# Kernel optimization log

Measured on AMD Instinct MI355X. Metric: run time of the kernel, lower is better.

Reference implementation:

```python
import jax, jax.numpy as jnp
import numpy as np

LN_EPS = 1e-5


def _ln_all_nonbatch(t):
    # torch nn.LayerNorm(t.size()[1:]) created fresh each call: identity affine,
    # normalize jointly over all non-batch dims, biased variance, eps=1e-5.
    axes = tuple(range(1, t.ndim))
    mu = jnp.mean(t, axis=axes, keepdims=True)
    var = jnp.mean(jnp.square(t - mu), axis=axes, keepdims=True)
    return (t - mu) / jnp.sqrt(var + LN_EPS)


def setup_inputs() -> dict:
    key = jax.random.key(0)
    kx, kq, kk, kv = jax.random.split(key, 4)
    B, S, E, d = 32, 1024, 768, 64
    x = jax.random.normal(kx, (B, S, E), dtype=jnp.float32)
    Wq = jax.random.normal(kq, (E, d), dtype=jnp.float32)
    Wk = jax.random.normal(kk, (E, d), dtype=jnp.float32)
    Wv = jax.random.normal(kv, (E, d), dtype=jnp.float32)
    return {"x": x, "Wq": Wq, "Wk": Wk, "Wv": Wv}


def reference(x, Wq, Wk, Wv):
    # x: [B,S,E]; Wq/Wk/Wv: [E,d]
    Q = jnp.einsum('bse,ed->bsd', x, Wq)            # [B,S,d]
    K = jnp.swapaxes(jnp.einsum('bse,ed->bsd', x, Wk), -2, -1)  # [B,d,S]
    V = jnp.einsum('bse,ed->bsd', x, Wv)            # [B,S,d]
    Q = _ln_all_nonbatch(Q)
    K = _ln_all_nonbatch(K)
    V = _ln_all_nonbatch(V)
    d = Q.shape[-1]  # K.shape[1] after transpose == head dim
    scores = jnp.einsum('bsd,bdt->bst', Q, K) / jnp.sqrt(jnp.float32(d))  # [B,S,S]
    attn = jax.nn.softmax(scores, axis=-1)
    return jnp.einsum('bst,btd->bsd', attn, V)      # [B,S,d]
```

## Files before the change

### kernel.cpp

```cpp
#include <hip/hip_runtime.h>
#include <hip/hip_fp16.h>

typedef _Float16 f16x8 __attribute__((ext_vector_type(8)));
typedef _Float16 f16x4 __attribute__((ext_vector_type(4)));
typedef float    f32x4 __attribute__((ext_vector_type(4)));

#define NB   32
#define SEQ  1024
#define EDIM 768
#define HD   64
#define MTOT (NB * SEQ)

__global__ __launch_bounds__(256) void pack_w(const float* __restrict__ Wq,
                                              const float* __restrict__ Wk,
                                              const float* __restrict__ Wv,
                                              _Float16* __restrict__ Wt) {
    int c = blockIdx.x;
    const float* src = (c < 64) ? Wq : (c < 128) ? Wk : Wv;
    int cc = c & 63;
    for (int e = threadIdx.x; e < EDIM; e += 256)
        Wt[(size_t)c * EDIM + e] = (_Float16)src[(size_t)e * HD + cc];
}

__global__ __launch_bounds__(256) void proj_kernel(const float* __restrict__ x,
                                                   const _Float16* __restrict__ Wt,
                                                   _Float16* __restrict__ q16,
                                                   _Float16* __restrict__ k16,
                                                   _Float16* __restrict__ v16,
                                                   float* __restrict__ part,
                                                   float* __restrict__ ksum) {
    __shared__ _Float16 xs[2][64][72];
    __shared__ _Float16 wsh[2][192][72];
    __shared__ float red[4][6];
    const int tid  = threadIdx.x;
    const int wave = tid >> 6, lane = tid & 63;
    const int lr = lane & 15, lk = (lane >> 4) * 8, lrow = (lane >> 4) * 4;
    const int m0 = blockIdx.x * 64;

    f32x4 acc[12] = {};
    f32x4 xv[4];
    f16x8 wv[6];

    #pragma unroll
    for (int i = 0; i < 4; ++i) {
        int lin = tid + i * 256, r = lin >> 4, c4 = (lin & 15) * 4;
        xv[i] = *(const f32x4*)&x[(size_t)(m0 + r) * EDIM + c4];
    }
    #pragma unroll
    for (int i = 0; i < 6; ++i) {
        int lin = tid + i * 256, c = lin >> 3, c8 = (lin & 7) * 8;
        wv[i] = *(const f16x8*)&Wt[(size_t)c * EDIM + c8];
    }
    #pragma unroll
    for (int i = 0; i < 4; ++i) {
        int lin = tid + i * 256, r = lin >> 4, c4 = (lin & 15) * 4;
        f16x4 h;
        h[0] = (_Float16)xv[i][0]; h[1] = (_Float16)xv[i][1];
        h[2] = (_Float16)xv[i][2]; h[3] = (_Float16)xv[i][3];
        *(f16x4*)&xs[0][r][c4] = h;
    }
    #pragma unroll
    for (int i = 0; i < 6; ++i) {
        int lin = tid + i * 256, c = lin >> 3, c8 = (lin & 7) * 8;
        *(f16x8*)&wsh[0][c][c8] = wv[i];
    }
    __syncthreads();

    for (int kt = 0; kt < 12; ++kt) {
        const int cur = kt & 1;
        if (kt < 11) {
            const int e0 = (kt + 1) * 64;
            #pragma unroll
            for (int i = 0; i < 4; ++i) {
                int lin = tid + i * 256, r = lin >> 4, c4 = (lin & 15) * 4;
                xv[i] = *(const f32x4*)&x[(size_t)(m0 + r) * EDIM + e0 + c4];
            }
            #pragma unroll
            for (int i = 0; i < 6; ++i) {
                int lin = tid + i * 256, c = lin >> 3, c8 = (lin & 7) * 8;
                wv[i] = *(const f16x8*)&Wt[(size_t)c * EDIM + e0 + c8];
            }
        }
        f16x8 a0  = *(const f16x8*)&xs[cur][wave * 16 + lr][lk];
        f16x8 a0b = *(const f16x8*)&xs[cur][wave * 16 + lr][32 + lk];
        #pragma unroll
        for (int nb = 0; nb < 12; ++nb) {
            f16x8 b0 = *(const f16x8*)&wsh[cur][nb * 16 + lr][lk];
            f16x8 b1 = *(const f16x8*)&wsh[cur][nb * 16 + lr][32 + lk];
            acc[nb] = __builtin_amdgcn_mfma_f32_16x16x32_f16(a0,  b0, acc[nb], 0, 0, 0);
            acc[nb] = __builtin_amdgcn_mfma_f32_16x16x32_f16(a0b, b1, acc[nb], 0, 0, 0);
        }
        if (kt < 11) {
            #pragma unroll
            for (int i = 0; i < 4; ++i) {
                int lin = tid + i * 256, r = lin >> 4, c4 = (lin & 15) * 4;
                f16x4 h;
                h[0] = (_Float16)xv[i][0]; h[1] = (_Float16)xv[i][1];
                h[2] = (_Float16)xv[i][2]; h[3] = (_Float16)xv[i][3];
                *(f16x4*)&xs[cur ^ 1][r][c4] = h;
            }
            #pragma unroll
            for (int i = 0; i < 6; ++i) {
                int lin = tid + i * 256, c = lin >> 3, c8 = (lin & 7) * 8;
                *(f16x8*)&wsh[cur ^ 1][c][c8] = wv[i];
            }
            __syncthreads();
        }
    }

    #pragma unroll
    for (int nb = 0; nb < 12; ++nb) {
        _Float16* dst = (nb < 4) ? q16 : (nb < 8) ? k16 : v16;
        int lc = (nb & 3) * 16 + lr;
        #pragma unroll
        for (int j = 0; j < 4; ++j)
            dst[(size_t)(m0 + wave * 16 + lrow + j) * HD + lc] = (_Float16)acc[nb][j];
    }

    #pragma unroll
    for (int j = 0; j < 4; ++j) {
        float ks = (acc[4][j] + acc[5][j]) + (acc[6][j] + acc[7][j]);
        ks += __shfl_xor(ks, 1); ks += __shfl_xor(ks, 2);
        ks += __shfl_xor(ks, 4); ks += __shfl_xor(ks, 8);
        if (lr == 0) ksum[m0 + wave * 16 + lrow + j] = ks;
    }

    #pragma unroll
    for (int t3 = 0; t3 < 3; ++t3) {
        float s = 0.f, q = 0.f;
        #pragma unroll
        for (int nb = t3 * 4; nb < t3 * 4 + 4; ++nb)
            #pragma unroll
            for (int j = 0; j < 4; ++j) { float v = acc[nb][j]; s += v; q += v * v; }
        #pragma unroll
        for (int off = 1; off < 64; off <<= 1) {
            s += __shfl_xor(s, off); q += __shfl_xor(q, off);
        }
        if (lane == 0) { red[wave][t3 * 2] = s; red[wave][t3 * 2 + 1] = q; }
    }
    __syncthreads();
    if (tid < 6)
        part[blockIdx.x * 6 + tid] = red[0][tid] + red[1][tid] + red[2][tid] + red[3][tid];
}

__global__ __launch_bounds__(64) void stats_reduce(const float* __restrict__ part,
                                                   float* __restrict__ stats) {
    int b = blockIdx.x, a = threadIdx.x;
    if (a < 3) {
        double s = 0.0, q = 0.0;
        for (int i = 0; i < 16; ++i) {
            s += (double)part[(b * 16 + i) * 6 + a * 2];
            q += (double)part[(b * 16 + i) * 6 + a * 2 + 1];
        }
        double mean = s / 65536.0;
        double var  = q / 65536.0 - mean * mean;
        stats[b * 8 + a * 2 + 0] = (float)mean;
        stats[b * 8 + a * 2 + 1] = (float)(1.0 / sqrt(var + 1e-5));
    }
}

__global__ __launch_bounds__(256) void transpose_v(const _Float16* __restrict__ v16,
                                                   _Float16* __restrict__ v16t) {
    __shared__ _Float16 t[64][72];
    int b = blockIdx.x >> 4, s0 = (blockIdx.x & 15) * 64;
    int tid = threadIdx.x;
    for (int i = 0; i < 2; ++i) {
        int lin = tid + i * 256;
        int s = lin >> 3, d8 = (lin & 7) * 8;
        *(f16x8*)&t[s][d8] = *(const f16x8*)&v16[((size_t)b * SEQ + s0 + s) * HD + d8];
    }
    __syncthreads();
    for (int i = 0; i < 2; ++i) {
        int lin = tid + i * 256;
        int d = lin >> 3, s8 = (lin & 7) * 8;
        f16x8 g;
        for (int k = 0; k < 8; ++k) g[k] = t[s8 + k][d];
        *(f16x8*)&v16t[((size_t)b * HD + d) * SEQ + s0 + s8] = g;
    }
}

__global__ __launch_bounds__(256) void attn_kernel(const _Float16* __restrict__ q16,
                                                   const _Float16* __restrict__ k16,
                                                   const _Float16* __restrict__ v16t,
                                                   const float* __restrict__ stats,
                                                   const float* __restrict__ ksum,
                                                   float* __restrict__ out) {
    __shared__ _Float16 ksm[64][72];
    __shared__ _Float16 vsm[64][72];
    __shared__ _Float16 psm[4][16][72];
    const int d_ = blockIdx.x;
    const int b = (d_ & 7) * 4 + ((d_ >> 3) & 3), qt = d_ >> 5;
    const int tid = threadIdx.x, wave = tid >> 6, lane = tid & 63;
    const int lr = lane & 15, lk = (lane >> 4) * 8, lrow = (lane >> 4) * 4;
    const float sscale = stats[b * 8 + 1] * stats[b * 8 + 3] * 0.125f;
    const float adjscale = sscale * stats[b * 8 + 0];
    const float mv = stats[b * 8 + 4], rv = stats[b * 8 + 5];
    const int q0 = qt * 64 + wave * 16;
    const _Float16* Qb = q16 + ((size_t)b * SEQ + q0) * HD;
    const float* ksb = ksum + b * SEQ;

    f16x8 aq0 = *(const f16x8*)&Qb[(size_t)lr * HD + lk];
    f16x8 aq1 = *(const f16x8*)&Qb[(size_t)lr * HD + 32 + lk];

    f32x4 o[4] = {};
    float mrow[4], lsum[4];
    for (int j = 0; j < 4; ++j) { mrow[j] = -1e30f; lsum[j] = 0.f; }

    for (int kv0 = 0; kv0 < SEQ; kv0 += 64) {
        for (int i = 0; i < 2; ++i) {
            int lin = tid + i * 256;
            int r = lin >> 3, c = (lin & 7) * 8;
            *(f16x8*)&ksm[r][c] = *(const f16x8*)&k16[((size_t)b * SEQ + kv0 + r) * HD + c];
        }
        for (int i = 0; i < 2; ++i) {
            int lin = tid + i * 256;
            int dd = lin >> 3, c = (lin & 7) * 8;
            *(f16x8*)&vsm[dd][c] = *(const f16x8*)&v16t[((size_t)b * HD + dd) * SEQ + kv0 + c];
        }
        __syncthreads();

        f32x4 sa[4];
        float adjv[4];
        for (int cb = 0; cb < 4; ++cb) {
            sa[cb] = (f32x4){0.f, 0.f, 0.f, 0.f};
            f16x8 bk0 = *(const f16x8*)&ksm[cb * 16 + lr][lk];
            f16x8 bk1 = *(const f16x8*)&ksm[cb * 16 + lr][32 + lk];
            sa[cb] = __builtin_amdgcn_mfma_f32_16x16x32_f16(aq0, bk0, sa[cb], 0, 0, 0);
            sa[cb] = __builtin_amdgcn_mfma_f32_16x16x32_f16(aq1, bk1, sa[cb], 0, 0, 0);
            adjv[cb] = adjscale * ksb[kv0 + cb * 16 + lr];
        }

        for (int j = 0; j < 4; ++j) {
            float sv0 = sa[0][j] * sscale - adjv[0];
            float sv1 = sa[1][j] * sscale - adjv[1];
            float sv2 = sa[2][j] * sscale - adjv[2];
            float sv3 = sa[3][j] * sscale - adjv[3];
            float pm = fmaxf(fmaxf(sv0, sv1), fmaxf(sv2, sv3));
            pm = fmaxf(pm, __shfl_xor(pm, 1));
            pm = fmaxf(pm, __shfl_xor(pm, 2));
            pm = fmaxf(pm, __shfl_xor(pm, 4));
            pm = fmaxf(pm, __shfl_xor(pm, 8));
            float mnew  = fmaxf(mrow[j], pm);
            float alpha = __expf(mrow[j] - mnew);
            mrow[j] = mnew;
            float p0 = __expf(sv0 - mnew), p1 = __expf(sv1 - mnew);
            float p2 = __expf(sv2 - mnew), p3 = __expf(sv3 - mnew);
            sa[0][j] = p0; sa[1][j] = p1; sa[2][j] = p2; sa[3][j] = p3;
            float rs = (p0 + p1) + (p2 + p3);
            rs += __shfl_xor(rs, 1); rs += __shfl_xor(rs, 2);
            rs += __shfl_xor(rs, 4); rs += __shfl_xor(rs, 8);
            lsum[j] = lsum[j] * alpha + rs;
            o[0][j] *= alpha; o[1][j] *= alpha; o[2][j] *= alpha; o[3][j] *= alpha;
        }
        for (int cb = 0; cb < 4; ++cb)
            for (int j = 0; j < 4; ++j)
                psm[wave][lrow + j][cb * 16 + lr] = (_Float16)sa[cb][j];

        f16x8 pa0 = *(const f16x8*)&psm[wave][lr][lk];
        f16x8 pa1 = *(const f16x8*)&psm[wave][lr][32 + lk];
        for (int db = 0; db < 4; ++db) {
            f16x8 bv0 = *(const f16x8*)&vsm[db * 16 + lr][lk];
            f16x8 bv1 = *(const f16x8*)&vsm[db * 16 + lr][32 + lk];
            o[db] = __builtin_amdgcn_mfma_f32_16x16x32_f16(pa0, bv0, o[db], 0, 0, 0);
            o[db] = __builtin_amdgcn_mfma_f32_16x16x32_f16(pa1, bv1, o[db], 0, 0, 0);
        }
        __syncthreads();
    }

    for (int j = 0; j < 4; ++j) {
        float inv = 1.f / lsum[j];
        size_t row = (size_t)b * SEQ + q0 + lrow + j;
        for (int db = 0; db < 4; ++db)
            out[row * HD + db * 16 + lr] = rv * (o[db][j] * inv - mv);
    }
}

extern "C" void kernel_launch(void* const* d_in, const int* in_sizes, int n_in,
                              void* d_out, int out_size, void* d_ws, size_t ws_size,
                              hipStream_t stream) {
    const float* x  = (const float*)d_in[0];
    const float* Wq = (const float*)d_in[1];
    const float* Wk = (const float*)d_in[2];
    const float* Wv = (const float*)d_in[3];
    float* out = (float*)d_out;
    char* ws = (char*)d_ws;

    _Float16* Wt   = (_Float16*)ws;
    float* stats   = (float*)(ws + 0x50000);
    float* ksum    = (float*)(ws + 0x51000);
    float* part    = (float*)(ws + 0x72000);
    _Float16* q16  = (_Float16*)(ws + 0x100000);
    _Float16* k16  = (_Float16*)(ws + 0x500000);
    _Float16* v16  = (_Float16*)(ws + 0x900000);
    _Float16* v16t = (_Float16*)(ws + 0xD00000);

    pack_w<<<192, 256, 0, stream>>>(Wq, Wk, Wv, Wt);
    proj_kernel<<<MTOT / 64, 256, 0, stream>>>(x, Wt, q16, k16, v16, part, ksum);
    stats_reduce<<<NB, 64, 0, stream>>>(part, stats);
    transpose_v<<<NB * 16, 256, 0, stream>>>(v16, v16t);
    attn_kernel<<<NB * 16, 256, 0, stream>>>(q16, k16, v16t, stats, ksum, out);
}
```

Baseline: 77.21 us.

## Fuse V transpose into projection, enlarge proj tile, register-prefetch K/V in attention

The projection kernel now handles 128 rows per block. It loads x straight from global memory into MFMA A fragments instead of staging it through shared memory, and it writes V directly in transposed layout, so the separate transpose_v kernel and its launch are gone. The attention kernel keeps K fragments in registers, loaded straight from global, and double-buffers the next K/V tile with a manually unrolled step macro. It also folds log2e into the scale so it can use exp2f. In exchange, register pressure goes up, the projection grid has half as many blocks (fewer waves to fill the GPU), and the V writes are strided.

```diff
diff --git a/kernel.cpp b/kernel.cpp
--- a/kernel.cpp
+++ b/kernel.cpp
@@ -10,6 +10,7 @@
 #define EDIM 768
 #define HD   64
 #define MTOT (NB * SEQ)
+#define LOG2E 1.44269504088896340736f
 
 __global__ __launch_bounds__(256) void pack_w(const float* __restrict__ Wq,
                                               const float* __restrict__ Wk,
@@ -26,40 +27,32 @@
                                                    const _Float16* __restrict__ Wt,
                                                    _Float16* __restrict__ q16,
                                                    _Float16* __restrict__ k16,
-                                                   _Float16* __restrict__ v16,
+                                                   _Float16* __restrict__ v16t,
                                                    float* __restrict__ part,
                                                    float* __restrict__ ksum) {
-    __shared__ _Float16 xs[2][64][72];
     __shared__ _Float16 wsh[2][192][72];
     __shared__ float red[4][6];
-    const int tid  = threadIdx.x;
-    const int wave = tid >> 6, lane = tid & 63;
+    const int tid = threadIdx.x, wave = tid >> 6, lane = tid & 63;
     const int lr = lane & 15, lk = (lane >> 4) * 8, lrow = (lane >> 4) * 4;
-    const int m0 = blockIdx.x * 64;
-
-    f32x4 acc[12] = {};
-    f32x4 xv[4];
+    const int m0 = blockIdx.x * 128;
+    const int bb = blockIdx.x >> 3;
+    const float* xr0 = x + (size_t)(m0 + wave * 32 + lr) * EDIM;
+    const float* xr1 = xr0 + (size_t)16 * EDIM;
+
+    f32x4 acc[2][12] = {};
+    f32x4 xv[8];
     f16x8 wv[6];
 
-    #pragma unroll
-    for (int i = 0; i < 4; ++i) {
-        int lin = tid + i * 256, r = lin >> 4, c4 = (lin & 15) * 4;
-        xv[i] = *(const f32x4*)&x[(size_t)(m0 + r) * EDIM + c4];
-    }
+    xv[0] = *(const f32x4*)&xr0[lk];      xv[1] = *(const f32x4*)&xr0[lk + 4];
+    xv[2] = *(const f32x4*)&xr0[32 + lk]; xv[3] = *(const f32x4*)&xr0[36 + lk];
+    xv[4] = *(const f32x4*)&xr1[lk];      xv[5] = *(const f32x4*)&xr1[lk + 4];
+    xv[6] = *(const f32x4*)&xr1[32 + lk]; xv[7] = *(const f32x4*)&xr1[36 + lk];
     #pragma unroll
     for (int i = 0; i < 6; ++i) {
         int lin = tid + i * 256, c = lin >> 3, c8 = (lin & 7) * 8;
         wv[i] = *(const f16x8*)&Wt[(size_t)c * EDIM + c8];
     }
     #pragma unroll
-    for (int i = 0; i < 4; ++i) {
-        int lin = tid + i * 256, r = lin >> 4, c4 = (lin & 15) * 4;
-        f16x4 h;
-        h[0] = (_Float16)xv[i][0]; h[1] = (_Float16)xv[i][1];
-        h[2] = (_Float16)xv[i][2]; h[3] = (_Float16)xv[i][3];
-        *(f16x4*)&xs[0][r][c4] = h;
-    }
-    #pragma unroll
     for (int i = 0; i < 6; ++i) {
         int lin = tid + i * 256, c = lin >> 3, c8 = (lin & 7) * 8;
         *(f16x8*)&wsh[0][c][c8] = wv[i];
@@ -68,37 +61,36 @@
 
     for (int kt = 0; kt < 12; ++kt) {
         const int cur = kt & 1;
+        f16x8 a00, a01, a10, a11;
+        #pragma unroll
+        for (int j = 0; j < 4; ++j) {
+            a00[j] = (_Float16)xv[0][j]; a00[4 + j] = (_Float16)xv[1][j];
+            a01[j] = (_Float16)xv[2][j]; a01[4 + j] = (_Float16)xv[3][j];
+            a10[j] = (_Float16)xv[4][j]; a10[4 + j] = (_Float16)xv[5][j];
+            a11[j] = (_Float16)xv[6][j]; a11[4 + j] = (_Float16)xv[7][j];
+        }
         if (kt < 11) {
             const int e0 = (kt + 1) * 64;
-            #pragma unroll
-            for (int i = 0; i < 4; ++i) {
-                int lin = tid + i * 256, r = lin >> 4, c4 = (lin & 15) * 4;
-                xv[i] = *(const f32x4*)&x[(size_t)(m0 + r) * EDIM + e0 + c4];
-            }
+            xv[0] = *(const f32x4*)&xr0[e0 + lk];      xv[1] = *(const f32x4*)&xr0[e0 + lk + 4];
+            xv[2] = *(const f32x4*)&xr0[e0 + 32 + lk]; xv[3] = *(const f32x4*)&xr0[e0 + 36 + lk];
+            xv[4] = *(const f32x4*)&xr1[e0 + lk];      xv[5] = *(const f32x4*)&xr1[e0 + lk + 4];
+            xv[6] = *(const f32x4*)&xr1[e0 + 32 + lk]; xv[7] = *(const f32x4*)&xr1[e0 + 36 + lk];
             #pragma unroll
             for (int i = 0; i < 6; ++i) {
                 int lin = tid + i * 256, c = lin >> 3, c8 = (lin & 7) * 8;
                 wv[i] = *(const f16x8*)&Wt[(size_t)c * EDIM + e0 + c8];
             }
         }
-        f16x8 a0  = *(const f16x8*)&xs[cur][wave * 16 + lr][lk];
-        f16x8 a0b = *(const f16x8*)&xs[cur][wave * 16 + lr][32 + lk];
         #pragma unroll
         for (int nb = 0; nb < 12; ++nb) {
             f16x8 b0 = *(const f16x8*)&wsh[cur][nb * 16 + lr][lk];
             f16x8 b1 = *(const f16x8*)&wsh[cur][nb * 16 + lr][32 + lk];
-            acc[nb] = __builtin_amdgcn_mfma_f32_16x16x32_f16(a0,  b0, acc[nb], 0, 0, 0);
-            acc[nb] = __builtin_amdgcn_mfma_f32_16x16x32_f16(a0b, b1, acc[nb], 0, 0, 0);
+            acc[0][nb] = __builtin_amdgcn_mfma_f32_16x16x32_f16(a00, b0, acc[0][nb], 0, 0, 0);
+            acc[0][nb] = __builtin_amdgcn_mfma_f32_16x16x32_f16(a01, b1, acc[0][nb], 0, 0, 0);
+            acc[1][nb] = __builtin_amdgcn_mfma_f32_16x16x32_f16(a10, b0, acc[1][nb], 0, 0, 0);
+            acc[1][nb] = __builtin_amdgcn_mfma_f32_16x16x32_f16(a11, b1, acc[1][nb], 0, 0, 0);
         }
         if (kt < 11) {
-            #pragma unroll
-            for (int i = 0; i < 4; ++i) {
-                int lin = tid + i * 256, r = lin >> 4, c4 = (lin & 15) * 4;
-                f16x4 h;
-                h[0] = (_Float16)xv[i][0]; h[1] = (_Float16)xv[i][1];
-                h[2] = (_Float16)xv[i][2]; h[3] = (_Float16)xv[i][3];
-                *(f16x4*)&xs[cur ^ 1][r][c4] = h;
-            }
             #pragma unroll
             for (int i = 0; i < 6; ++i) {
                 int lin = tid + i * 256, c = lin >> 3, c8 = (lin & 7) * 8;
@@ -108,30 +100,44 @@
         }
     }
 
-    #pragma unroll
-    for (int nb = 0; nb < 12; ++nb) {
-        _Float16* dst = (nb < 4) ? q16 : (nb < 8) ? k16 : v16;
-        int lc = (nb & 3) * 16 + lr;
-        #pragma unroll
-        for (int j = 0; j < 4; ++j)
-            dst[(size_t)(m0 + wave * 16 + lrow + j) * HD + lc] = (_Float16)acc[nb][j];
-    }
-
-    #pragma unroll
-    for (int j = 0; j < 4; ++j) {
-        float ks = (acc[4][j] + acc[5][j]) + (acc[6][j] + acc[7][j]);
-        ks += __shfl_xor(ks, 1); ks += __shfl_xor(ks, 2);
-        ks += __shfl_xor(ks, 4); ks += __shfl_xor(ks, 8);
-        if (lr == 0) ksum[m0 + wave * 16 + lrow + j] = ks;
+    const int rowin0 = (m0 & 1023) + wave * 32;
+    #pragma unroll
+    for (int rg = 0; rg < 2; ++rg) {
+        const int rbase = m0 + wave * 32 + rg * 16 + lrow;
+        #pragma unroll
+        for (int nb = 0; nb < 8; ++nb) {
+            _Float16* dst = (nb < 4) ? q16 : k16;
+            int lc = (nb & 3) * 16 + lr;
+            #pragma unroll
+            for (int j = 0; j < 4; ++j)
+                dst[(size_t)(rbase + j) * HD + lc] = (_Float16)acc[rg][nb][j];
+        }
+        #pragma unroll
+        for (int nb = 8; nb < 12; ++nb) {
+            int col = (nb & 3) * 16 + lr;
+            f16x4 h;
+            #pragma unroll
+            for (int j = 0; j < 4; ++j) h[j] = (_Float16)acc[rg][nb][j];
+            *(f16x4*)&v16t[((size_t)(bb * 64 + col)) * SEQ + rowin0 + rg * 16 + lrow] = h;
+        }
+        #pragma unroll
+        for (int j = 0; j < 4; ++j) {
+            float ks = (acc[rg][4][j] + acc[rg][5][j]) + (acc[rg][6][j] + acc[rg][7][j]);
+            ks += __shfl_xor(ks, 1); ks += __shfl_xor(ks, 2);
+            ks += __shfl_xor(ks, 4); ks += __shfl_xor(ks, 8);
+            if (lr == 0) ksum[rbase + j] = ks;
+        }
     }
 
     #pragma unroll
     for (int t3 = 0; t3 < 3; ++t3) {
         float s = 0.f, q = 0.f;
         #pragma unroll
-        for (int nb = t3 * 4; nb < t3 * 4 + 4; ++nb)
-            #pragma unroll
-            for (int j = 0; j < 4; ++j) { float v = acc[nb][j]; s += v; q += v * v; }
+        for (int rg = 0; rg < 2; ++rg)
+            #pragma unroll
+            for (int nb = t3 * 4; nb < t3 * 4 + 4; ++nb)
+                #pragma unroll
+                for (int j = 0; j < 4; ++j) { float v = acc[rg][nb][j]; s += v; q += v * v; }
         #pragma unroll
         for (int off = 1; off < 64; off <<= 1) {
             s += __shfl_xor(s, off); q += __shfl_xor(q, off);
@@ -148,9 +154,9 @@
     int b = blockIdx.x, a = threadIdx.x;
     if (a < 3) {
         double s = 0.0, q = 0.0;
-        for (int i = 0; i < 16; ++i) {
-            s += (double)part[(b * 16 + i) * 6 + a * 2];
-            q += (double)part[(b * 16 + i) * 6 + a * 2 + 1];
+        for (int i = 0; i < 8; ++i) {
+            s += (double)part[(b * 8 + i) * 6 + a * 2];
+            q += (double)part[(b * 8 + i) * 6 + a * 2 + 1];
         }
         double mean = s / 65536.0;
         double var  = q / 65536.0 - mean * mean;
@@ -159,25 +165,67 @@
     }
 }
 
-__global__ __launch_bounds__(256) void transpose_v(const _Float16* __restrict__ v16,
-                                                   _Float16* __restrict__ v16t) {
-    __shared__ _Float16 t[64][72];
-    int b = blockIdx.x >> 4, s0 = (blockIdx.x & 15) * 64;
-    int tid = threadIdx.x;
-    for (int i = 0; i < 2; ++i) {
-        int lin = tid + i * 256;
-        int s = lin >> 3, d8 = (lin & 7) * 8;
-        *(f16x8*)&t[s][d8] = *(const f16x8*)&v16[((size_t)b * SEQ + s0 + s) * HD + d8];
-    }
-    __syncthreads();
-    for (int i = 0; i < 2; ++i) {
-        int lin = tid + i * 256;
-        int d = lin >> 3, s8 = (lin & 7) * 8;
-        f16x8 g;
-        for (int k = 0; k < 8; ++k) g[k] = t[s8 + k][d];
-        *(f16x8*)&v16t[((size_t)b * HD + d) * SEQ + s0 + s8] = g;
-    }
-}
+#define ATTN_STEP(KFC, KFN, VVN, T, PRE)                                              \
+  {                                                                                   \
+    if (PRE) {                                                                        \
+      const int kvn = ((T) + 1) * 64;                                                 \
+      _Pragma("unroll")                                                               \
+      for (int cb = 0; cb < 4; ++cb) {                                                \
+        KFN[cb * 2]     = *(const f16x8*)&Kb[(size_t)(kvn + cb * 16 + lr) * HD + lk]; \
+        KFN[cb * 2 + 1] = *(const f16x8*)&Kb[(size_t)(kvn + cb * 16 + lr) * HD + 32 + lk]; \
+      }                                                                               \
+      _Pragma("unroll")                                                               \
+      for (int i = 0; i < 2; ++i) { int lin = tid + i * 256;                          \
+        VVN[i] = *(const f16x8*)&Vtb[(size_t)(lin >> 3) * SEQ + kvn + (lin & 7) * 8]; } \
+    }                                                                                 \
+    f32x4 sa[4]; float adjv[4];                                                       \
+    _Pragma("unroll")                                                                 \
+    for (int cb = 0; cb < 4; ++cb) {                                                  \
+      sa[cb] = (f32x4){0.f, 0.f, 0.f, 0.f};                                           \
+      sa[cb] = __builtin_amdgcn_mfma_f32_16x16x32_f16(aq0, KFC[cb * 2],     sa[cb], 0, 0, 0); \
+      sa[cb] = __builtin_amdgcn_mfma_f32_16x16x32_f16(aq1, KFC[cb * 2 + 1], sa[cb], 0, 0, 0); \
+      adjv[cb] = adjscale * ksb[(T) * 64 + cb * 16 + lr];                             \
+    }                                                                                 \
+    _Pragma("unroll")                                                                 \
+    for (int j = 0; j < 4; ++j) {                                                     \
+      float sv0 = sa[0][j] * sscale - adjv[0], sv1 = sa[1][j] * sscale - adjv[1];     \
+      float sv2 = sa[2][j] * sscale - adjv[2], sv3 = sa[3][j] * sscale - adjv[3];     \
+      float pm = fmaxf(fmaxf(sv0, sv1), fmaxf(sv2, sv3));                             \
+      pm = fmaxf(pm, __shfl_xor(pm, 1)); pm = fmaxf(pm, __shfl_xor(pm, 2));           \
+      pm = fmaxf(pm, __shfl_xor(pm, 4)); pm = fmaxf(pm, __shfl_xor(pm, 8));           \
+      float mnew = fmaxf(mrow[j], pm);                                                \
+      float alpha = exp2f(mrow[j] - mnew); mrow[j] = mnew;                            \
+      float p0 = exp2f(sv0 - mnew), p1 = exp2f(sv1 - mnew);                           \
+      float p2 = exp2f(sv2 - mnew), p3 = exp2f(sv3 - mnew);                           \
+      sa[0][j] = p0; sa[1][j] = p1; sa[2][j] = p2; sa[3][j] = p3;                     \
+      float rs = (p0 + p1) + (p2 + p3);                                               \
+      rs += __shfl_xor(rs, 1); rs += __shfl_xor(rs, 2);                               \
+      rs += __shfl_xor(rs, 4); rs += __shfl_xor(rs, 8);                               \
+      lsum[j] = lsum[j] * alpha + rs;                                                 \
+      o[0][j] *= alpha; o[1][j] *= alpha; o[2][j] *= alpha; o[3][j] *= alpha;         \
+    }                                                                                 \
+    _Pragma("unroll")                                                                 \
+    for (int cb = 0; cb < 4; ++cb)                                                    \
+      _Pragma("unroll")                                                               \
+      for (int j = 0; j < 4; ++j)                                                     \
+        psm[wave][lrow + j][cb * 16 + lr] = (_Float16)sa[cb][j];                      \
+    f16x8 pa0 = *(const f16x8*)&psm[wave][lr][lk];                                    \
+    f16x8 pa1 = *(const f16x8*)&psm[wave][lr][32 + lk];                               \
+    _Pragma("unroll")                                                                 \
+    for (int db = 0; db < 4; ++db) {                                                  \
+      f16x8 bv0 = *(const f16x8*)&vsm[db * 16 + lr][lk];                              \
+      f16x8 bv1 = *(const f16x8*)&vsm[db * 16 + lr][32 + lk];                         \
+      o[db] = __builtin_amdgcn_mfma_f32_16x16x32_f16(pa0, bv0, o[db], 0, 0, 0);       \
+      o[db] = __builtin_amdgcn_mfma_f32_16x16x32_f16(pa1, bv1, o[db], 0, 0, 0);       \
+    }                                                                                 \
+    if (PRE) {                                                                        \
+      __syncthreads();                                                                \
+      _Pragma("unroll")                                                               \
+      for (int i = 0; i < 2; ++i) { int lin = tid + i * 256;                          \
+        *(f16x8*)&vsm[lin >> 3][(lin & 7) * 8] = VVN[i]; }                            \
+      __syncthreads();                                                                \
+    }                                                                                 \
+  }
 
 __global__ __launch_bounds__(256) void attn_kernel(const _Float16* __restrict__ q16,
                                                    const _Float16* __restrict__ k16,
@@ -185,91 +233,59 @@
                                                    const float* __restrict__ stats,
                                                    const float* __restrict__ ksum,
                                                    float* __restrict__ out) {
-    __shared__ _Float16 ksm[64][72];
     __shared__ _Float16 vsm[64][72];
     __shared__ _Float16 psm[4][16][72];
     const int d_ = blockIdx.x;
     const int b = (d_ & 7) * 4 + ((d_ >> 3) & 3), qt = d_ >> 5;
     const int tid = threadIdx.x, wave = tid >> 6, lane = tid & 63;
     const int lr = lane & 15, lk = (lane >> 4) * 8, lrow = (lane >> 4) * 4;
-    const float sscale = stats[b * 8 + 1] * stats[b * 8 + 3] * 0.125f;
+    const float sscale = stats[b * 8 + 1] * stats[b * 8 + 3] * 0.125f * LOG2E;
     const float adjscale = sscale * stats[b * 8 + 0];
     const float mv = stats[b * 8 + 4], rv = stats[b * 8 + 5];
     const int q0 = qt * 64 + wave * 16;
-    const _Float16* Qb = q16 + ((size_t)b * SEQ + q0) * HD;
+    const _Float16* Qb  = q16 + ((size_t)b * SEQ + q0) * HD;
+    const _Float16* Kb  = k16 + (size_t)b * SEQ * HD;
+    const _Float16* Vtb = v16t + (size_t)b * HD * SEQ;
     const float* ksb = ksum + b * SEQ;
 
     f16x8 aq0 = *(const f16x8*)&Qb[(size_t)lr * HD + lk];
     f16x8 aq1 = *(const f16x8*)&Qb[(size_t)lr * HD + 32 + lk];
 
+    f16x8 kfA[8], kfB[8], vvA[2], vvB[2];
     f32x4 o[4] = {};
     float mrow[4], lsum[4];
+    #pragma unroll
     for (int j = 0; j < 4; ++j) { mrow[j] = -1e30f; lsum[j] = 0.f; }
 
-    for (int kv0 = 0; kv0 < SEQ; kv0 += 64) {
-        for (int i = 0; i < 2; ++i) {
-            int lin = tid + i * 256;
-            int r = lin >> 3, c = (lin & 7) * 8;
-            *(f16x8*)&ksm[r][c] = *(const f16x8*)&k16[((size_t)b * SEQ + kv0 + r) * HD + c];
-        }
-        for (int i = 0; i < 2; ++i) {
-            int lin = tid + i * 256;
-            int dd = lin >> 3, c = (lin & 7) * 8;
-            *(f16x8*)&vsm[dd][c] = *(const f16x8*)&v16t[((size_t)b * HD + dd) * SEQ + kv0 + c];
-        }
-        __syncthreads();
-
-        f32x4 sa[4];
-        float adjv[4];
-        for (int cb = 0; cb < 4; ++cb) {
-            sa[cb] = (f32x4){0.f, 0.f, 0.f, 0.f};
-            f16x8 bk0 = *(const f16x8*)&ksm[cb * 16 + lr][lk];
-            f16x8 bk1 = *(const f16x8*)&ksm[cb * 16 + lr][32 + lk];
-            sa[cb] = __builtin_amdgcn_mfma_f32_16x16x32_f16(aq0, bk0, sa[cb], 0, 0, 0);
-            sa[cb] = __builtin_amdgcn_mfma_f32_16x16x32_f16(aq1, bk1, sa[cb], 0, 0, 0);
-            adjv[cb] = adjscale * ksb[kv0 + cb * 16 + lr];
-        }
-
-        for (int j = 0; j < 4; ++j) {
-            float sv0 = sa[0][j] * sscale - adjv[0];
-            float sv1 = sa[1][j] * sscale - adjv[1];
-            float sv2 = sa[2][j] * sscale - adjv[2];
-            float sv3 = sa[3][j] * sscale - adjv[3];
-            float pm = fmaxf(fmaxf(sv0, sv1), fmaxf(sv2, sv3));
-            pm = fmaxf(pm, __shfl_xor(pm, 1));
-            pm = fmaxf(pm, __shfl_xor(pm, 2));
-            pm = fmaxf(pm, __shfl_xor(pm, 4));
-            pm = fmaxf(pm, __shfl_xor(pm, 8));
-            float mnew  = fmaxf(mrow[j], pm);
-            float alpha = __expf(mrow[j] - mnew);
-            mrow[j] = mnew;
-            float p0 = __expf(sv0 - mnew), p1 = __expf(sv1 - mnew);
-            float p2 = __expf(sv2 - mnew), p3 = __expf(sv3 - mnew);
-            sa[0][j] = p0; sa[1][j] = p1; sa[2][j] = p2; sa[3][j] = p3;
-            float rs = (p0 + p1) + (p2 + p3);
-            rs += __shfl_xor(rs, 1); rs += __shfl_xor(rs, 2);
-            rs += __shfl_xor(rs, 4); rs += __shfl_xor(rs, 8);
-            lsum[j] = lsum[j] * alpha + rs;
-            o[0][j] *= alpha; o[1][j] *= alpha; o[2][j] *= alpha; o[3][j] *= alpha;
-        }
-        for (int cb = 0; cb < 4; ++cb)
-            for (int j = 0; j < 4; ++j)
-                psm[wave][lrow + j][cb * 16 + lr] = (_Float16)sa[cb][j];
-
-        f16x8 pa0 = *(const f16x8*)&psm[wave][lr][lk];
-        f16x8 pa1 = *(const f16x8*)&psm[wave][lr][32 + lk];
-        for (int db = 0; db < 4; ++db) {
-            f16x8 bv0 = *(const f16x8*)&vsm[db * 16 + lr][lk];
-            f16x8 bv1 = *(const f16x8*)&vsm[db * 16 + lr][32 + lk];
-            o[db] = __builtin_amdgcn_mfma_f32_16x16x32_f16(pa0, bv0, o[db], 0, 0, 0);
-            o[db] = __builtin_amdgcn_mfma_f32_16x16x32_f16(pa1, bv1, o[db], 0, 0, 0);
-        }
-        __syncthreads();
-    }
-
+    #pragma unroll
+    for (int cb = 0; cb < 4; ++cb) {
+        kfA[cb * 2]     = *(const f16x8*)&Kb[(size_t)(cb * 16 + lr) * HD + lk];
+        kfA[cb * 2 + 1] = *(const f16x8*)&Kb[(size_t)(cb * 16 + lr) * HD + 32 + lk];
+    }
+    #pragma unroll
+    for (int i = 0; i < 2; ++i) {
+        int lin = tid + i * 256;
+        vvA[i] = *(const f16x8*)&Vtb[(size_t)(lin >> 3) * SEQ + (lin & 7) * 8];
+    }
+    #pragma unroll
+    for (int i = 0; i < 2; ++i) {
+        int lin = tid + i * 256;
+        *(f16x8*)&vsm[lin >> 3][(lin & 7) * 8] = vvA[i];
+    }
+    __syncthreads();
+
+    for (int t2 = 0; t2 < 7; ++t2) {
+        ATTN_STEP(kfA, kfB, vvB, 2 * t2,     1);
+        ATTN_STEP(kfB, kfA, vvA, 2 * t2 + 1, 1);
+    }
+    ATTN_STEP(kfA, kfB, vvB, 14, 1);
+    ATTN_STEP(kfB, kfA, vvA, 15, 0);
+
+    #pragma unroll
     for (int j = 0; j < 4; ++j) {
         float inv = 1.f / lsum[j];
         size_t row = (size_t)b * SEQ + q0 + lrow + j;
+        #pragma unroll
         for (int db = 0; db < 4; ++db)
             out[row * HD + db * 16 + lr] = rv * (o[db][j] * inv - mv);
     }
@@ -291,12 +307,10 @@
     float* part    = (float*)(ws + 0x72000);
     _Float16* q16  = (_Float16*)(ws + 0x100000);
     _Float16* k16  = (_Float16*)(ws + 0x500000);
-    _Float16* v16  = (_Float16*)(ws + 0x900000);
-    _Float16* v16t = (_Float16*)(ws + 0xD00000);
+    _Float16* v16t = (_Float16*)(ws + 0x900000);
 
     pack_w<<<192, 256, 0, stream>>>(Wq, Wk, Wv, Wt);
-    proj_kernel<<<MTOT / 64, 256, 0, stream>>>(x, Wt, q16, k16, v16, part, ksum);
+    proj_kernel<<<MTOT / 128, 256, 0, stream>>>(x, Wt, q16, k16, v16t, part, ksum);
     stats_reduce<<<NB, 64, 0, stream>>>(part, stats);
-    transpose_v<<<NB * 16, 256, 0, stream>>>(v16, v16t);
     attn_kernel<<<NB * 16, 256, 0, stream>>>(q16, k16, v16t, stats, ksum, out);
 }
```

Measured after the change: 89.65 us. 16.1% more time.

## Drop LDS staging in projection, write V transposed directly, use exp2 softmax

Applied to the files above, without the earlier changes.

The projection kernel stops staging x and W tiles through shared memory. Each wave now loads its own x rows and the W fragments straight from global memory, which leaves only one barrier in the kernel. V is written already transposed from the projection epilogue, so the separate transpose_v kernel and its extra memory round trip are removed. The attention kernel folds log2(e) into the score scale so it can use exp2f, and several of its loops get explicit unroll pragmas. In exchange, W fragments are re-read from global or L2 by every wave with no LDS reuse, and the strided transposed V stores may coalesce poorly.

```diff
diff --git a/kernel.cpp b/kernel.cpp
--- a/kernel.cpp
+++ b/kernel.cpp
@@ -10,6 +10,7 @@
 #define EDIM 768
 #define HD   64
 #define MTOT (NB * SEQ)
+#define LOG2E 1.44269504088896340736f
 
 __global__ __launch_bounds__(256) void pack_w(const float* __restrict__ Wq,
                                               const float* __restrict__ Wk,
@@ -26,105 +27,70 @@
                                                    const _Float16* __restrict__ Wt,
                                                    _Float16* __restrict__ q16,
                                                    _Float16* __restrict__ k16,
-                                                   _Float16* __restrict__ v16,
+                                                   _Float16* __restrict__ v16t,
                                                    float* __restrict__ part,
                                                    float* __restrict__ ksum) {
-    __shared__ _Float16 xs[2][64][72];
-    __shared__ _Float16 wsh[2][192][72];
     __shared__ float red[4][6];
-    const int tid  = threadIdx.x;
-    const int wave = tid >> 6, lane = tid & 63;
+    const int tid = threadIdx.x, wave = tid >> 6, lane = tid & 63;
     const int lr = lane & 15, lk = (lane >> 4) * 8, lrow = (lane >> 4) * 4;
     const int m0 = blockIdx.x * 64;
+    const int bb = m0 >> 10;
+    const float* xr = x + (size_t)(m0 + wave * 16 + lr) * EDIM;
 
     f32x4 acc[12] = {};
     f32x4 xv[4];
-    f16x8 wv[6];
-
-    #pragma unroll
-    for (int i = 0; i < 4; ++i) {
-        int lin = tid + i * 256, r = lin >> 4, c4 = (lin & 15) * 4;
-        xv[i] = *(const f32x4*)&x[(size_t)(m0 + r) * EDIM + c4];
-    }
-    #pragma unroll
-    for (int i = 0; i < 6; ++i) {
-        int lin = tid + i * 256, c = lin >> 3, c8 = (lin & 7) * 8;
-        wv[i] = *(const f16x8*)&Wt[(size_t)c * EDIM + c8];
-    }
-    #pragma unroll
-    for (int i = 0; i < 4; ++i) {
-        int lin = tid + i * 256, r = lin >> 4, c4 = (lin & 15) * 4;
+
+    xv[0] = *(const f32x4*)&xr[lk];      xv[1] = *(const f32x4*)&xr[lk + 4];
+    xv[2] = *(const f32x4*)&xr[32 + lk]; xv[3] = *(const f32x4*)&xr[36 + lk];
+
+    for (int kt = 0; kt < 12; ++kt) {
+        const int e0 = kt * 64;
+        f16x8 a00, a01;
+        #pragma unroll
+        for (int j = 0; j < 4; ++j) {
+            a00[j] = (_Float16)xv[0][j]; a00[4 + j] = (_Float16)xv[1][j];
+            a01[j] = (_Float16)xv[2][j]; a01[4 + j] = (_Float16)xv[3][j];
+        }
+        if (kt < 11) {
+            const int e1 = e0 + 64;
+            xv[0] = *(const f32x4*)&xr[e1 + lk];      xv[1] = *(const f32x4*)&xr[e1 + lk + 4];
+            xv[2] = *(const f32x4*)&xr[e1 + 32 + lk]; xv[3] = *(const f32x4*)&xr[e1 + 36 + lk];
+        }
+        #pragma unroll
+        for (int nb = 0; nb < 12; ++nb) {
+            const _Float16* wrow = &Wt[(size_t)(nb * 16 + lr) * EDIM + e0];
+            f16x8 b0 = *(const f16x8*)&wrow[lk];
+            f16x8 b1 = *(const f16x8*)&wrow[32 + lk];
+            acc[nb] = __builtin_amdgcn_mfma_f32_16x16x32_f16(a00, b0, acc[nb], 0, 0, 0);
+            acc[nb] = __builtin_amdgcn_mfma_f32_16x16x32_f16(a01, b1, acc[nb], 0, 0, 0);
+        }
+    }
+
+    const int rbase = m0 + wave * 16 + lrow;
+    const int rowin = (m0 & 1023) + wave * 16 + lrow;
+    #pragma unroll
+    for (int nb = 0; nb < 8; ++nb) {
+        _Float16* dst = (nb < 4) ? q16 : k16;
+        int lc = (nb & 3) * 16 + lr;
+        #pragma unroll
+        for (int j = 0; j < 4; ++j)
+            dst[(size_t)(rbase + j) * HD + lc] = (_Float16)acc[nb][j];
+    }
+    #pragma unroll
+    for (int nb = 8; nb < 12; ++nb) {
+        int col = (nb & 3) * 16 + lr;
         f16x4 h;
-        h[0] = (_Float16)xv[i][0]; h[1] = (_Float16)xv[i][1];
-        h[2] = (_Float16)xv[i][2]; h[3] = (_Float16)xv[i][3];
-        *(f16x4*)&xs[0][r][c4] = h;
-    }
-    #pragma unroll
-    for (int i = 0; i < 6; ++i) {
-        int lin = tid + i * 256, c = lin >> 3, c8 = (lin & 7) * 8;
-        *(f16x8*)&wsh[0][c][c8] = wv[i];
-    }
-    __syncthreads();
-
-    for (int kt = 0; kt < 12; ++kt) {
-        const int cur = kt & 1;
-        if (kt < 11) {
-            const int e0 = (kt + 1) * 64;
-            #pragma unroll
-            for (int i = 0; i < 4; ++i) {
-                int lin = tid + i * 256, r = lin >> 4, c4 = (lin & 15) * 4;
-                xv[i] = *(const f32x4*)&x[(size_t)(m0 + r) * EDIM + e0 + c4];
-            }
-            #pragma unroll
-            for (int i = 0; i < 6; ++i) {
-                int lin = tid + i * 256, c = lin >> 3, c8 = (lin & 7) * 8;
-                wv[i] = *(const f16x8*)&Wt[(size_t)c * EDIM + e0 + c8];
-            }
-        }
-        f16x8 a0  = *(const f16x8*)&xs[cur][wave * 16 + lr][lk];
-        f16x8 a0b = *(const f16x8*)&xs[cur][wave * 16 + lr][32 + lk];
-        #pragma unroll
-        for (int nb = 0; nb < 12; ++nb) {
-            f16x8 b0 = *(const f16x8*)&wsh[cur][nb * 16 + lr][lk];
-            f16x8 b1 = *(const f16x8*)&wsh[cur][nb * 16 + lr][32 + lk];
-            acc[nb] = __builtin_amdgcn_mfma_f32_16x16x32_f16(a0,  b0, acc[nb], 0, 0, 0);
-            acc[nb] = __builtin_amdgcn_mfma_f32_16x16x32_f16(a0b, b1, acc[nb], 0, 0, 0);
-        }
-        if (kt < 11) {
-            #pragma unroll
-            for (int i = 0; i < 4; ++i) {
-                int lin = tid + i * 256, r = lin >> 4, c4 = (lin & 15) * 4;
-                f16x4 h;
-                h[0] = (_Float16)xv[i][0]; h[1] = (_Float16)xv[i][1];
-                h[2] = (_Float16)xv[i][2]; h[3] = (_Float16)xv[i][3];
-                *(f16x4*)&xs[cur ^ 1][r][c4] = h;
-            }
-            #pragma unroll
-            for (int i = 0; i < 6; ++i) {
-                int lin = tid + i * 256, c = lin >> 3, c8 = (lin & 7) * 8;
-                *(f16x8*)&wsh[cur ^ 1][c][c8] = wv[i];
-            }
-            __syncthreads();
-        }
-    }
-
-    #pragma unroll
-    for (int nb = 0; nb < 12; ++nb) {
-        _Float16* dst = (nb < 4) ? q16 : (nb < 8) ? k16 : v16;
-        int lc = (nb & 3) * 16 + lr;
-        #pragma unroll
-        for (int j = 0; j < 4; ++j)
-            dst[(size_t)(m0 + wave * 16 + lrow + j) * HD + lc] = (_Float16)acc[nb][j];
-    }
-
+        #pragma unroll
+        for (int j = 0; j < 4; ++j) h[j] = (_Float16)acc[nb][j];
+        *(f16x4*)&v16t[((size_t)(bb * 64 + col)) * SEQ + rowin] = h;
+    }
     #pragma unroll
     for (int j = 0; j < 4; ++j) {
         float ks = (acc[4][j] + acc[5][j]) + (acc[6][j] + acc[7][j]);
         ks += __shfl_xor(ks, 1); ks += __shfl_xor(ks, 2);
         ks += __shfl_xor(ks, 4); ks += __shfl_xor(ks, 8);
-        if (lr == 0) ksum[m0 + wave * 16 + lrow + j] = ks;
-    }
-
+        if (lr == 0) ksum[rbase + j] = ks;
+    }
     #pragma unroll
     for (int t3 = 0; t3 < 3; ++t3) {
         float s = 0.f, q = 0.f;
@@ -156,26 +122,6 @@
         double var  = q / 65536.0 - mean * mean;
         stats[b * 8 + a * 2 + 0] = (float)mean;
         stats[b * 8 + a * 2 + 1] = (float)(1.0 / sqrt(var + 1e-5));
-    }
-}
-
-__global__ __launch_bounds__(256) void transpose_v(const _Float16* __restrict__ v16,
-                                                   _Float16* __restrict__ v16t) {
-    __shared__ _Float16 t[64][72];
-    int b = blockIdx.x >> 4, s0 = (blockIdx.x & 15) * 64;
-    int tid = threadIdx.x;
-    for (int i = 0; i < 2; ++i) {
-        int lin = tid + i * 256;
-        int s = lin >> 3, d8 = (lin & 7) * 8;
-        *(f16x8*)&t[s][d8] = *(const f16x8*)&v16[((size_t)b * SEQ + s0 + s) * HD + d8];
-    }
-    __syncthreads();
-    for (int i = 0; i < 2; ++i) {
-        int lin = tid + i * 256;
-        int d = lin >> 3, s8 = (lin & 7) * 8;
-        f16x8 g;
-        for (int k = 0; k < 8; ++k) g[k] = t[s8 + k][d];
-        *(f16x8*)&v16t[((size_t)b * HD + d) * SEQ + s0 + s8] = g;
     }
 }
 
@@ -192,7 +138,7 @@
     const int b = (d_ & 7) * 4 + ((d_ >> 3) & 3), qt = d_ >> 5;
     const int tid = threadIdx.x, wave = tid >> 6, lane = tid & 63;
     const int lr = lane & 15, lk = (lane >> 4) * 8, lrow = (lane >> 4) * 4;
-    const float sscale = stats[b * 8 + 1] * stats[b * 8 + 3] * 0.125f;
+    const float sscale = stats[b * 8 + 1] * stats[b * 8 + 3] * 0.125f * LOG2E;
     const float adjscale = sscale * stats[b * 8 + 0];
     const float mv = stats[b * 8 + 4], rv = stats[b * 8 + 5];
     const int q0 = qt * 64 + wave * 16;
@@ -204,6 +150,7 @@
 
     f32x4 o[4] = {};
     float mrow[4], lsum[4];
+    #pragma unroll
     for (int j = 0; j < 4; ++j) { mrow[j] = -1e30f; lsum[j] = 0.f; }
 
     for (int kv0 = 0; kv0 < SEQ; kv0 += 64) {
@@ -221,6 +168,7 @@
 
         f32x4 sa[4];
         float adjv[4];
+        #pragma unroll
         for (int cb = 0; cb < 4; ++cb) {
             sa[cb] = (f32x4){0.f, 0.f, 0.f, 0.f};
             f16x8 bk0 = *(const f16x8*)&ksm[cb * 16 + lr][lk];
@@ -230,6 +178,7 @@
             adjv[cb] = adjscale * ksb[kv0 + cb * 16 + lr];
         }
 
+        #pragma unroll
         for (int j = 0; j < 4; ++j) {
             float sv0 = sa[0][j] * sscale - adjv[0];
             float sv1 = sa[1][j] * sscale - adjv[1];
@@ -241,10 +190,10 @@
             pm = fmaxf(pm, __shfl_xor(pm, 4));
             pm = fmaxf(pm, __shfl_xor(pm, 8));
             float mnew  = fmaxf(mrow[j], pm);
-            float alpha = __expf(mrow[j] - mnew);
+            float alpha = exp2f(mrow[j] - mnew);
             mrow[j] = mnew;
-            float p0 = __expf(sv0 - mnew), p1 = __expf(sv1 - mnew);
-            float p2 = __expf(sv2 - mnew), p3 = __expf(sv3 - mnew);
+            float p0 = exp2f(sv0 - mnew), p1 = exp2f(sv1 - mnew);
+            float p2 = exp2f(sv2 - mnew), p3 = exp2f(sv3 - mnew);
             sa[0][j] = p0; sa[1][j] = p1; sa[2][j] = p2; sa[3][j] = p3;
             float rs = (p0 + p1) + (p2 + p3);
             rs += __shfl_xor(rs, 1); rs += __shfl_xor(rs, 2);
@@ -252,12 +201,15 @@
             lsum[j] = lsum[j] * alpha + rs;
             o[0][j] *= alpha; o[1][j] *= alpha; o[2][j] *= alpha; o[3][j] *= alpha;
         }
+        #pragma unroll
         for (int cb = 0; cb < 4; ++cb)
+            #pragma unroll
             for (int j = 0; j < 4; ++j)
                 psm[wave][lrow + j][cb * 16 + lr] = (_Float16)sa[cb][j];
 
         f16x8 pa0 = *(const f16x8*)&psm[wave][lr][lk];
         f16x8 pa1 = *(const f16x8*)&psm[wave][lr][32 + lk];
+        #pragma unroll
         for (int db = 0; db < 4; ++db) {
             f16x8 bv0 = *(const f16x8*)&vsm[db * 16 + lr][lk];
             f16x8 bv1 = *(const f16x8*)&vsm[db * 16 + lr][32 + lk];
@@ -267,9 +219,11 @@
         __syncthreads();
     }
 
+    #pragma unroll
     for (int j = 0; j < 4; ++j) {
         float inv = 1.f / lsum[j];
         size_t row = (size_t)b * SEQ + q0 + lrow + j;
+        #pragma unroll
         for (int db = 0; db < 4; ++db)
             out[row * HD + db * 16 + lr] = rv * (o[db][j] * inv - mv);
     }
@@ -291,12 +245,10 @@
     float* part    = (float*)(ws + 0x72000);
     _Float16* q16  = (_Float16*)(ws + 0x100000);
     _Float16* k16  = (_Float16*)(ws + 0x500000);
-    _Float16* v16  = (_Float16*)(ws + 0x900000);
-    _Float16* v16t = (_Float16*)(ws + 0xD00000);
+    _Float16* v16t = (_Float16*)(ws + 0x900000);
 
     pack_w<<<192, 256, 0, stream>>>(Wq, Wk, Wv, Wt);
-    proj_kernel<<<MTOT / 64, 256, 0, stream>>>(x, Wt, q16, k16, v16, part, ksum);
+    proj_kernel<<<MTOT / 64, 256, 0, stream>>>(x, Wt, q16, k16, v16t, part, ksum);
     stats_reduce<<<NB, 64, 0, stream>>>(part, stats);
-    transpose_v<<<NB * 16, 256, 0, stream>>>(v16, v16t);
     attn_kernel<<<NB * 16, 256, 0, stream>>>(q16, k16, v16t, stats, ksum, out);
 }
```

Result: slower. 129.3 us (+67.4%).
